# Kernel optimization log

Measured on AMD Instinct MI355X. Metric: run time of the kernel, lower is better.

Reference implementation:

```python
import jax, jax.numpy as jnp
import numpy as np

N_NODES = 50000
N_EDGES = 500000
IN_CH = 128
HID = 64
HEADS = 4
N_LAYERS = 3
OUT_CH = 16
N_GRAPHS = 64
NEG_SLOPE = 0.2  # PyG GATConv default


def setup_inputs() -> dict:
    key = jax.random.key(0)
    ks = jax.random.split(key, 20)
    inp = {
        'x': jax.random.normal(ks[0], (N_NODES, IN_CH), dtype=jnp.float32),
        'edge_attr': jax.random.normal(ks[1], (N_EDGES, 8), dtype=jnp.float32),
        'edge_index': jax.random.randint(ks[2], (2, N_EDGES), 0, N_NODES, dtype=jnp.int64),
        'batch': jnp.sort(jax.random.randint(ks[3], (N_NODES,), 0, N_GRAPHS, dtype=jnp.int64)),
    }
    kidx = 4
    in_dim = IN_CH
    for i in range(N_LAYERS):
        inp[f'W{i}'] = jax.random.normal(ks[kidx], (in_dim, HEADS * HID), dtype=jnp.float32) * (1.0 / np.sqrt(in_dim)); kidx += 1
        inp[f'asrc{i}'] = jax.random.normal(ks[kidx], (HEADS, HID), dtype=jnp.float32) * 0.1; kidx += 1
        inp[f'adst{i}'] = jax.random.normal(ks[kidx], (HEADS, HID), dtype=jnp.float32) * 0.1; kidx += 1
        inp[f'b{i}'] = jnp.zeros((HEADS * HID,), dtype=jnp.float32)
        in_dim = HEADS * HID
    inp['Wc'] = jax.random.normal(ks[kidx], (HEADS * HID, OUT_CH), dtype=jnp.float32) * (1.0 / np.sqrt(HEADS * HID)); kidx += 1
    inp['bc'] = jnp.zeros((OUT_CH,), dtype=jnp.float32)
    return inp


def _gat_layer(x, src, dst, W, asrc, adst, b):
    # x: [N, F_in] -> h: [N, H, C]
    N = x.shape[0]
    h = (x @ W).reshape(N, HEADS, HID)
    s_src = jnp.einsum('nhc,hc->nh', h, asrc)  # [N, H]
    s_dst = jnp.einsum('nhc,hc->nh', h, adst)
    e = jax.nn.leaky_relu(s_src[src] + s_dst[dst], NEG_SLOPE)  # [E, H]
    # segment softmax over incoming edges of each destination node
    m = jax.ops.segment_max(e, dst, num_segments=N)            # [N, H]
    ex = jnp.exp(e - m[dst])
    denom = jax.ops.segment_sum(ex, dst, num_segments=N)       # [N, H]
    alpha = ex / (denom[dst] + 1e-16)                           # [E, H]
    out = jax.ops.segment_sum(alpha[:, :, None] * h[src], dst, num_segments=N)  # [N, H, C]
    return out.reshape(N, HEADS * HID) + b


def reference(x, edge_attr, edge_index, batch,
              W0, asrc0, adst0, b0,
              W1, asrc1, adst1, b1,
              W2, asrc2, adst2, b2,
              Wc, bc):
    N = x.shape[0]
    loop = jnp.arange(N, dtype=edge_index.dtype)
    # PyG GATConv adds self-loops by default
    src = jnp.concatenate([edge_index[0], loop])
    dst = jnp.concatenate([edge_index[1], loop])
    params = [(W0, asrc0, adst0, b0), (W1, asrc1, adst1, b1), (W2, asrc2, adst2, b2)]
    h = x
    for (W, asrc, adst, b) in params:
        h = jax.nn.relu(_gat_layer(h, src, dst, W, asrc, adst, b))
        # nn.Dropout(0.5) is identity in eval mode
    pooled = jax.ops.segment_sum(h, batch, num_segments=N_GRAPHS)  # global_add_pool
    return pooled @ Wc + bc
```

## Files before the change

### kernel.cpp

```cpp
#include <hip/hip_runtime.h>
#include <hip/hip_bf16.h>

#define NNODES 50000
#define NEDGES 500000
#define INCH 128
#define HID 64
#define HEADS 4
#define FDIM 256
#define NGRAPHS 64
#define OUTCH 16
#define NEG_SLOPE 0.2f

#define BM 64
#define BN 256
#define BK 32

typedef float f32x4 __attribute__((ext_vector_type(4)));
typedef _Float16 f16x8 __attribute__((ext_vector_type(8)));
typedef _Float16 f16x4 __attribute__((ext_vector_type(4)));

__device__ inline void gld_lds16(const void* g, void* l) {
    __builtin_amdgcn_global_load_lds((__attribute__((address_space(1))) void*)g,
                                     (__attribute__((address_space(3))) void*)l, 16, 0, 0);
}


__global__ void k_hist(const int* __restrict__ dst, int E, int* __restrict__ counts) {
    int i = blockIdx.x * blockDim.x + threadIdx.x;
    if (i < E) atomicAdd(&counts[dst[i]], 1);
}

__global__ __launch_bounds__(256) void k_blocksum(const int* __restrict__ counts, int N,
                                                  int* __restrict__ bsum) {
    int idx = blockIdx.x * 256 + threadIdx.x;
    int v = (idx < N) ? counts[idx] : 0;
#pragma unroll
    for (int off = 32; off; off >>= 1) v += __shfl_xor(v, off);
    __shared__ int wsum[4];
    if ((threadIdx.x & 63) == 0) wsum[threadIdx.x >> 6] = v;
    __syncthreads();
    if (threadIdx.x == 0) bsum[blockIdx.x] = wsum[0] + wsum[1] + wsum[2] + wsum[3];
}

__global__ __launch_bounds__(256) void k_scanfinal(const int* __restrict__ counts,
                                                   const int* __restrict__ bsum, int N,
                                                   int* __restrict__ rowstart,
                                                   int* __restrict__ cursor) {
    __shared__ int tmp[256];
    __shared__ int wsum[4];
    int t = threadIdx.x, b = blockIdx.x;
    int p = 0;
    for (int i = t; i < b; i += 256) p += bsum[i];
#pragma unroll
    for (int off = 32; off; off >>= 1) p += __shfl_xor(p, off);
    int idx = b * 256 + t;
    int v = (idx < N) ? counts[idx] : 0;
    tmp[t] = v;
    if ((t & 63) == 0) wsum[t >> 6] = p;
    __syncthreads();
    int bp = wsum[0] + wsum[1] + wsum[2] + wsum[3];
    for (int off = 1; off < 256; off <<= 1) {
        int u = (t >= off) ? tmp[t - off] : 0;
        __syncthreads();
        tmp[t] += u;
        __syncthreads();
    }
    if (idx < N) {
        int incl = bp + tmp[t];
        rowstart[idx + 1] = incl;
        cursor[idx] = incl - v;
    }
    if (idx == 0) rowstart[0] = 0;
}

__global__ void k_scatter(const int* __restrict__ src, const int* __restrict__ dst, int E,
                          int* __restrict__ cursor, int* __restrict__ csr_src) {
    int i = blockIdx.x * blockDim.x + threadIdx.x;
    if (i < E) {
        int p = atomicAdd(&cursor[dst[i]], 1);
        csr_src[p] = src[i];
    }
}


__device__ inline void wdecomp_body(const float* __restrict__ W, _Float16* __restrict__ Wt,
                                    int K, int bb) {
    int i = bb * 256 + threadIdx.x;
    int k = i >> 8, n = i & 255;
    Wt[n * K + k] = (_Float16)W[i];
}

__global__ __launch_bounds__(256) void k_convert(
    const float* __restrict__ X, _Float16* __restrict__ Xf, int bx,
    const float* __restrict__ W0, _Float16* __restrict__ Wt0,
    const float* __restrict__ W1, _Float16* __restrict__ Wt1,
    const float* __restrict__ W2, _Float16* __restrict__ Wt2) {
    int b = blockIdx.x;
    if (b < bx) {
        int i = b * 256 + threadIdx.x;
        float4 v = ((const float4*)X)[i];
        f16x4 o = {(_Float16)v.x, (_Float16)v.y, (_Float16)v.z, (_Float16)v.w};
        ((f16x4*)Xf)[i] = o;
    } else if (b < bx + 128) {
        wdecomp_body(W0, Wt0, INCH, b - bx);
    } else if (b < bx + 384) {
        wdecomp_body(W1, Wt1, FDIM, b - bx - 128);
    } else {
        wdecomp_body(W2, Wt2, FDIM, b - bx - 384);
    }
}


__global__ __launch_bounds__(256) void k_gemm_mfma(
    const _Float16* __restrict__ A, const _Float16* __restrict__ B,
    const float* __restrict__ av, const float* __restrict__ dv,
    _Float16* __restrict__ Hf,
    float* __restrict__ ssrcO, float* __restrict__ sdstO, int M, int K) {
    __shared__ _Float16 sA[2][BM * BK];
    __shared__ _Float16 sB[2][BN * BK];

    const int t = threadIdx.x;
    const int row0 = blockIdx.x * BM;
    const int wv = t >> 6, ln = t & 63, lr = ln & 15, lk = ln >> 4;

    const int ar = wv * 16 + (ln >> 2);
    const int alc = (ln & 3) ^ ((ar >> 1) & 3);
    const size_t agoff = (size_t)min(row0 + ar, M - 1) * K + alc * 8;
    const int fsc = lk ^ ((lr >> 1) & 3);

    f32x4 acc[4][4] = {};
    const int nt = K / BK;

#define STAGE(tt, p)                                                        \
    do {                                                                    \
        int _k0 = (tt)*BK;                                                  \
        gld_lds16(A + agoff + _k0, &sA[p][wv * 512]);                       \
        _Pragma("unroll") for (int _j = 0; _j < 4; ++_j) {                  \
            int _br = _j * 64 + ar;                                         \
            gld_lds16(B + (size_t)_br * K + _k0 + alc * 8,                  \
                      &sB[p][_j * 2048 + wv * 512]);                        \
        }                                                                   \
    } while (0)

    STAGE(0, 0);
    __syncthreads();
    for (int tt = 0; tt < nt; ++tt) {
        int cur = tt & 1;
        if (tt + 1 < nt) STAGE(tt + 1, cur ^ 1);

        f16x8 af[4];
#pragma unroll
        for (int mi = 0; mi < 4; ++mi)
            af[mi] = *(const f16x8*)&sA[cur][(mi * 16 + lr) * BK + fsc * 8];
#pragma unroll
        for (int ni = 0; ni < 4; ++ni) {
            f16x8 bf = *(const f16x8*)&sB[cur][(wv * 64 + ni * 16 + lr) * BK + fsc * 8];
#pragma unroll
            for (int mi = 0; mi < 4; ++mi)
                acc[mi][ni] = __builtin_amdgcn_mfma_f32_16x16x32_f16(af[mi], bf, acc[mi][ni], 0, 0, 0);
        }
        __syncthreads();
    }
#undef STAGE

    float ps[4][4] = {}, pd[4][4] = {};
#pragma unroll
    for (int ni = 0; ni < 4; ++ni) {
        int col = wv * 64 + ni * 16 + lr;
        float a_s = av[col], a_d = dv[col];
#pragma unroll
        for (int mi = 0; mi < 4; ++mi) {
            f32x4 v = acc[mi][ni];
            int r = row0 + mi * 16 + lk * 4;
#pragma unroll
            for (int j = 0; j < 4; ++j) {
                if (r + j < M) Hf[(size_t)(r + j) * FDIM + col] = (_Float16)v[j];
                ps[mi][j] += v[j] * a_s;
                pd[mi][j] += v[j] * a_d;
            }
        }
    }
#pragma unroll
    for (int mi = 0; mi < 4; ++mi) {
#pragma unroll
        for (int j = 0; j < 4; ++j) {
            float s = ps[mi][j], q = pd[mi][j];
            s += __shfl_xor(s, 1); s += __shfl_xor(s, 2);
            s += __shfl_xor(s, 4); s += __shfl_xor(s, 8);
            q += __shfl_xor(q, 1); q += __shfl_xor(q, 2);
            q += __shfl_xor(q, 4); q += __shfl_xor(q, 8);
            if (lr == 0) {
                int r = row0 + mi * 16 + lk * 4 + j;
                if (r < M) {
                    ssrcO[r * HEADS + wv] = s;
                    sdstO[r * HEADS + wv] = q;
                }
            }
        }
    }
}


__global__ __launch_bounds__(256) void k_aggregate(
    const _Float16* __restrict__ hf,
    const float* __restrict__ ssrc, const float* __restrict__ sdst,
    const int* __restrict__ rowstart, const int* __restrict__ csr_src,
    const float* __restrict__ bias,
    _Float16* __restrict__ outf, int N) {
    int wv = threadIdx.x >> 6, ln = threadIdx.x & 63;
    int n = blockIdx.x * 4 + wv;
    if (n >= N) return;
    int head = ln >> 4;
    int fo = head * 64 + (ln & 15) * 4;
    float sd = sdst[n * HEADS + head];
    float e = ssrc[n * HEADS + head] + sd;
    e = (e > 0.f) ? e : NEG_SLOPE * e;
    float m = e, d = 1.0f;
    f16x4 sv = *(const f16x4*)&hf[(size_t)n * FDIM + fo];
    float4 acc = make_float4((float)sv[0], (float)sv[1], (float)sv[2], (float)sv[3]);
    int r0 = rowstart[n], r1 = rowstart[n + 1];
    int cnt = r1 - r0;
    for (int base = 0; base < cnt; base += 16) {
        int s[16];
        f16x4 u[16];
        float c[16], w[16];
#pragma unroll
        for (int i = 0; i < 16; ++i) s[i] = csr_src[min(r0 + base + i, r1 - 1)];
#pragma unroll
        for (int i = 0; i < 16; ++i) u[i] = *(const f16x4*)&hf[(size_t)s[i] * FDIM + fo];
#pragma unroll
        for (int i = 0; i < 16; ++i) {
            float sc = ssrc[s[i] * HEADS + head] + sd;
            sc = (sc > 0.f) ? sc : NEG_SLOPE * sc;
            c[i] = (base + i < cnt) ? sc : -1e30f;
        }
        float mx = c[0];
#pragma unroll
        for (int i = 1; i < 16; ++i) mx = fmaxf(mx, c[i]);
        float mn = fmaxf(m, mx);
        float wa = __expf(m - mn);
#pragma unroll
        for (int i = 0; i < 16; ++i) w[i] = __expf(c[i] - mn);
        float sx = 0.f, sy = 0.f, sz = 0.f, sw = 0.f, sdn = 0.f;
#pragma unroll
        for (int i = 0; i < 16; ++i) {
            sx += w[i] * (float)u[i][0];
            sy += w[i] * (float)u[i][1];
            sz += w[i] * (float)u[i][2];
            sw += w[i] * (float)u[i][3];
            sdn += w[i];
        }
        acc.x = acc.x * wa + sx;
        acc.y = acc.y * wa + sy;
        acc.z = acc.z * wa + sz;
        acc.w = acc.w * wa + sw;
        d = d * wa + sdn;
        m = mn;
    }
    float inv = 1.0f / d;
    float4 bv = *(const float4*)&bias[fo];
    f16x4 o;
    o[0] = (_Float16)fmaxf(acc.x * inv + bv.x, 0.f);
    o[1] = (_Float16)fmaxf(acc.y * inv + bv.y, 0.f);
    o[2] = (_Float16)fmaxf(acc.z * inv + bv.z, 0.f);
    o[3] = (_Float16)fmaxf(acc.w * inv + bv.w, 0.f);
    *(f16x4*)&outf[(size_t)n * FDIM + fo] = o;
}


__global__ __launch_bounds__(256) void k_pool(const _Float16* __restrict__ hf,
                                              const int* __restrict__ batch,
                                              float* __restrict__ pooled, int N) {
    int f = threadIdx.x;
    int n0 = blockIdx.x * 128;
    if (n0 >= N) return;
    int n1 = min(n0 + 128, N);
    int g = batch[n0];
    float run = 0.f;
    for (int n = n0; n < n1; ++n) {
        int gn = batch[n];
        if (gn != g) {
            atomicAdd(&pooled[g * FDIM + f], run);
            run = 0.f;
            g = gn;
        }
        run += (float)hf[(size_t)n * FDIM + f];
    }
    atomicAdd(&pooled[g * FDIM + f], run);
}


__global__ __launch_bounds__(256) void k_final(const float* __restrict__ pooled,
                                               const float* __restrict__ Wc,
                                               const float* __restrict__ bc,
                                               float* __restrict__ out) {
    int tid = blockIdx.x * 256 + threadIdx.x;
    int g = tid >> 4, o = tid & 15;
    float s = bc[o];
    for (int k = 0; k < FDIM; ++k) s += pooled[g * FDIM + k] * Wc[k * OUTCH + o];
    out[g * OUTCH + o] = s;
}


extern "C" void kernel_launch(void* const* d_in, const int* in_sizes, int n_in,
                              void* d_out, int out_size, void* d_ws, size_t ws_size,
                              hipStream_t stream) {
    const float* x = (const float*)d_in[0];
    const int* edge_index = (const int*)d_in[2];
    const int* batch = (const int*)d_in[3];
    const float* W[3]    = {(const float*)d_in[4], (const float*)d_in[8],  (const float*)d_in[12]};
    const float* asrc[3] = {(const float*)d_in[5], (const float*)d_in[9],  (const float*)d_in[13]};
    const float* adst[3] = {(const float*)d_in[6], (const float*)d_in[10], (const float*)d_in[14]};
    const float* bias[3] = {(const float*)d_in[7], (const float*)d_in[11], (const float*)d_in[15]};
    const float* Wc = (const float*)d_in[16];
    const float* bc = (const float*)d_in[17];

    const int N = in_sizes[3];
    const int E = in_sizes[2] / 2;
    const int* e_src = edge_index;
    const int* e_dst = edge_index + E;

    char* ws = (char*)d_ws;
    size_t off = 0;
    _Float16* hb = (_Float16*)(ws + off); off += (size_t)N * FDIM * 2;
    _Float16* xf = (_Float16*)(ws + off); off += (size_t)N * INCH * 2;
    _Float16* P  = (_Float16*)(ws + off); off += (size_t)N * FDIM * 2;
    float* ssrc = (float*)(ws + off); off += (size_t)N * HEADS * 4;
    float* sdst = (float*)(ws + off); off += (size_t)N * HEADS * 4;
    int* rowstart = (int*)(ws + off); off += ((size_t)(N + 1) * 4 + 255) / 256 * 256;
    int* counts = (int*)(ws + off); off += (size_t)N * 4;
    int* cursor = (int*)(ws + off); off += (size_t)N * 4;
    int* csr_src = (int*)(ws + off); off += (size_t)E * 4;
    float* pooled = (float*)(ws + off); off += (size_t)NGRAPHS * FDIM * 4;
    int* bsum = (int*)(ws + off); off += ((size_t)((N + 255) / 256) * 4 + 255) / 256 * 256;
    _Float16* Wt[3];
    int Ks[3] = {INCH, FDIM, FDIM};
    for (int l = 0; l < 3; ++l) {
        Wt[l] = (_Float16*)(ws + off); off += (size_t)256 * Ks[l] * 2;
    }

    const int nb = (N + 255) / 256;

    hipMemsetAsync(counts, 0, (size_t)N * 4, stream);
    k_hist<<<(E + 255) / 256, 256, 0, stream>>>(e_dst, E, counts);
    k_blocksum<<<nb, 256, 0, stream>>>(counts, N, bsum);
    k_scanfinal<<<nb, 256, 0, stream>>>(counts, bsum, N, rowstart, cursor);
    k_scatter<<<(E + 255) / 256, 256, 0, stream>>>(e_src, e_dst, E, cursor, csr_src);

    {
        int bx = (N * INCH / 4) / 256;
        int btot = bx + (Ks[0] * 256) / 256 + (Ks[1] * 256) / 256 + (Ks[2] * 256) / 256;
        k_convert<<<btot, 256, 0, stream>>>(x, xf, bx, W[0], Wt[0], W[1], Wt[1], W[2], Wt[2]);
    }

    const _Float16* Af = xf;
    for (int l = 0; l < 3; ++l) {
        int K = Ks[l];
        k_gemm_mfma<<<(N + BM - 1) / BM, 256, 0, stream>>>(Af, Wt[l], asrc[l], adst[l],
                                                           hb, ssrc, sdst, N, K);
        k_aggregate<<<(N + 3) / 4, 256, 0, stream>>>(hb, ssrc, sdst, rowstart, csr_src,
                                                     bias[l], P, N);
        Af = P;
    }

    hipMemsetAsync(pooled, 0, (size_t)NGRAPHS * FDIM * 4, stream);
    k_pool<<<(N + 127) / 128, 256, 0, stream>>>(P, batch, pooled, N);
    k_final<<<4, 256, 0, stream>>>(pooled, Wc, bc, (float*)d_out);
}
```

Before: 384.3 us.

## Use persistent grid-stride waves and lane-parallel edge scores in GAT aggregation

The aggregation kernel becomes persistent: a fixed grid of 2048 blocks whose waves stride over nodes, replacing one wave per node with a grid of N/4 blocks. Each 16-lane head group now computes edge scores in parallel (one edge per lane), reduces max and sum through shuffles and broadcasts weights with __shfl. The edge chunk shrinks from 16 to 8. The intent is to cut redundant per-lane score and exp work and block launch overhead. The cost is extra shuffle traffic, fewer gathers in flight per chunk, and possible load imbalance across waves.

```diff
diff --git a/kernel.cpp b/kernel.cpp
--- a/kernel.cpp
+++ b/kernel.cpp
@@ -206,65 +206,66 @@
     const float* __restrict__ ssrc, const float* __restrict__ sdst,
     const int* __restrict__ rowstart, const int* __restrict__ csr_src,
     const float* __restrict__ bias,
-    _Float16* __restrict__ outf, int N) {
-    int wv = threadIdx.x >> 6, ln = threadIdx.x & 63;
-    int n = blockIdx.x * 4 + wv;
-    if (n >= N) return;
-    int head = ln >> 4;
-    int fo = head * 64 + (ln & 15) * 4;
-    float sd = sdst[n * HEADS + head];
-    float e = ssrc[n * HEADS + head] + sd;
-    e = (e > 0.f) ? e : NEG_SLOPE * e;
-    float m = e, d = 1.0f;
-    f16x4 sv = *(const f16x4*)&hf[(size_t)n * FDIM + fo];
-    float4 acc = make_float4((float)sv[0], (float)sv[1], (float)sv[2], (float)sv[3]);
-    int r0 = rowstart[n], r1 = rowstart[n + 1];
-    int cnt = r1 - r0;
-    for (int base = 0; base < cnt; base += 16) {
-        int s[16];
-        f16x4 u[16];
-        float c[16], w[16];
-#pragma unroll
-        for (int i = 0; i < 16; ++i) s[i] = csr_src[min(r0 + base + i, r1 - 1)];
-#pragma unroll
-        for (int i = 0; i < 16; ++i) u[i] = *(const f16x4*)&hf[(size_t)s[i] * FDIM + fo];
-#pragma unroll
-        for (int i = 0; i < 16; ++i) {
-            float sc = ssrc[s[i] * HEADS + head] + sd;
-            sc = (sc > 0.f) ? sc : NEG_SLOPE * sc;
-            c[i] = (base + i < cnt) ? sc : -1e30f;
-        }
-        float mx = c[0];
-#pragma unroll
-        for (int i = 1; i < 16; ++i) mx = fmaxf(mx, c[i]);
-        float mn = fmaxf(m, mx);
-        float wa = __expf(m - mn);
-#pragma unroll
-        for (int i = 0; i < 16; ++i) w[i] = __expf(c[i] - mn);
-        float sx = 0.f, sy = 0.f, sz = 0.f, sw = 0.f, sdn = 0.f;
-#pragma unroll
-        for (int i = 0; i < 16; ++i) {
-            sx += w[i] * (float)u[i][0];
-            sy += w[i] * (float)u[i][1];
-            sz += w[i] * (float)u[i][2];
-            sw += w[i] * (float)u[i][3];
-            sdn += w[i];
-        }
-        acc.x = acc.x * wa + sx;
-        acc.y = acc.y * wa + sy;
-        acc.z = acc.z * wa + sz;
-        acc.w = acc.w * wa + sw;
-        d = d * wa + sdn;
-        m = mn;
-    }
-    float inv = 1.0f / d;
+    _Float16* __restrict__ outf, int N, int nwaves) {
+    int wid = (blockIdx.x * blockDim.x + threadIdx.x) >> 6;
+    int ln = threadIdx.x & 63;
+    int head = ln >> 4, li = ln & 15;
+    int fo = head * 64 + li * 4;
     float4 bv = *(const float4*)&bias[fo];
-    f16x4 o;
-    o[0] = (_Float16)fmaxf(acc.x * inv + bv.x, 0.f);
-    o[1] = (_Float16)fmaxf(acc.y * inv + bv.y, 0.f);
-    o[2] = (_Float16)fmaxf(acc.z * inv + bv.z, 0.f);
-    o[3] = (_Float16)fmaxf(acc.w * inv + bv.w, 0.f);
-    *(f16x4*)&outf[(size_t)n * FDIM + fo] = o;
+
+    for (int n = wid; n < N; n += nwaves) {
+        float sd = sdst[n * HEADS + head];
+        float e = ssrc[n * HEADS + head] + sd;
+        e = (e > 0.f) ? e : NEG_SLOPE * e;
+        float m = e, d = 1.0f;
+        f16x4 sv = *(const f16x4*)&hf[(size_t)n * FDIM + fo];
+        float4 acc = make_float4((float)sv[0], (float)sv[1], (float)sv[2], (float)sv[3]);
+        int r0 = rowstart[n], r1 = rowstart[n + 1];
+        for (int base = r0; base < r1; base += 8) {
+            int s[8];
+#pragma unroll
+            for (int i = 0; i < 8; ++i) s[i] = csr_src[min(base + i, r1 - 1)];
+            float sc = -1e30f;
+            if (li < 8 && base + li < r1) {
+                sc = ssrc[s[li] * HEADS + head] + sd;
+                sc = (sc > 0.f) ? sc : NEG_SLOPE * sc;
+            }
+            float gmax = sc;
+#pragma unroll
+            for (int off = 1; off < 16; off <<= 1) gmax = fmaxf(gmax, __shfl_xor(gmax, off));
+            float mn = fmaxf(m, gmax);
+            float wl = __expf(sc - mn);
+            float wsum = wl;
+#pragma unroll
+            for (int off = 1; off < 16; off <<= 1) wsum += __shfl_xor(wsum, off);
+            f16x4 u[8];
+#pragma unroll
+            for (int i = 0; i < 8; ++i) u[i] = *(const f16x4*)&hf[(size_t)s[i] * FDIM + fo];
+            float wa = __expf(m - mn);
+            float sx = 0.f, sy = 0.f, sz = 0.f, sw = 0.f;
+#pragma unroll
+            for (int i = 0; i < 8; ++i) {
+                float wi = __shfl(wl, head * 16 + i);
+                sx += wi * (float)u[i][0];
+                sy += wi * (float)u[i][1];
+                sz += wi * (float)u[i][2];
+                sw += wi * (float)u[i][3];
+            }
+            acc.x = acc.x * wa + sx;
+            acc.y = acc.y * wa + sy;
+            acc.z = acc.z * wa + sz;
+            acc.w = acc.w * wa + sw;
+            d = d * wa + wsum;
+            m = mn;
+        }
+        float inv = 1.0f / d;
+        f16x4 o;
+        o[0] = (_Float16)fmaxf(acc.x * inv + bv.x, 0.f);
+        o[1] = (_Float16)fmaxf(acc.y * inv + bv.y, 0.f);
+        o[2] = (_Float16)fmaxf(acc.z * inv + bv.z, 0.f);
+        o[3] = (_Float16)fmaxf(acc.w * inv + bv.w, 0.f);
+        *(f16x4*)&outf[(size_t)n * FDIM + fo] = o;
+    }
 }
 
 
@@ -353,13 +354,15 @@
         k_convert<<<btot, 256, 0, stream>>>(x, xf, bx, W[0], Wt[0], W[1], Wt[1], W[2], Wt[2]);
     }
 
+    const int aggblocks = 2048;
+    const int nwaves = aggblocks * 4;
     const _Float16* Af = xf;
     for (int l = 0; l < 3; ++l) {
         int K = Ks[l];
         k_gemm_mfma<<<(N + BM - 1) / BM, 256, 0, stream>>>(Af, Wt[l], asrc[l], adst[l],
                                                            hb, ssrc, sdst, N, K);
-        k_aggregate<<<(N + 3) / 4, 256, 0, stream>>>(hb, ssrc, sdst, rowstart, csr_src,
-                                                     bias[l], P, N);
+        k_aggregate<<<aggblocks, 256, 0, stream>>>(hb, ssrc, sdst, rowstart, csr_src,
+                                                   bias[l], P, N, nwaves);
         Af = P;
     }
 
```

New measurement: 359.0 us. 6.6% less time.
